# Kernel tuning notes

Hardware: AMD Instinct MI355X
Metric: run time of the kernel (lower is better)

The kernel has to match this reference:

```python
import jax, jax.numpy as jnp
import numpy as np

N = 50000          # nodes
E = 1600000        # edges (avg degree 32)
B = 64             # graphs in batch
IN_CH = 128
HEADS = 8
HD = 8             # head_dim = ceil(64/8)
GH = HEADS * HD    # 64 = gat_hidden_dim
HIDDEN = 64
NC = 10
NEG_SLOPE = 0.2
BN_EPS = 1e-5
SIGMA = 0.5


def setup_inputs() -> dict:
    key = jax.random.key(0)
    ks = jax.random.split(key, 24)
    s = 0.1
    inp = {
        "x": jax.random.normal(ks[0], (N, IN_CH), jnp.float32),
        "raw_x": jax.random.uniform(ks[1], (N, 3), jnp.float32),
        "edge_index": jax.random.randint(ks[2], (2, E), 0, N, jnp.int32),
        "batch": jnp.sort(jax.random.randint(ks[3], (N,), 0, B, jnp.int32)),
        # conv1 (heads=8, out=8, edge_dim=1)
        "W1": jax.random.normal(ks[4], (IN_CH, GH), jnp.float32) * s,
        "att_src1": jax.random.normal(ks[5], (HEADS, HD), jnp.float32) * s,
        "att_dst1": jax.random.normal(ks[6], (HEADS, HD), jnp.float32) * s,
        "We1": jax.random.normal(ks[7], (1, GH), jnp.float32) * s,
        "att_e1": jax.random.normal(ks[8], (HEADS, HD), jnp.float32) * s,
        "b1": jax.random.normal(ks[9], (GH,), jnp.float32) * s,
        "gamma1": jnp.ones((GH,), jnp.float32),
        "beta1": jnp.zeros((GH,), jnp.float32),
        "rm1": jax.random.normal(ks[10], (GH,), jnp.float32) * s,
        "rv1": jax.random.uniform(ks[11], (GH,), jnp.float32) + 0.5,
        # conv2 (heads=1, out=64, edge_dim=1)
        "W2": jax.random.normal(ks[12], (GH, HIDDEN), jnp.float32) * s,
        "att_src2": jax.random.normal(ks[13], (1, HIDDEN), jnp.float32) * s,
        "att_dst2": jax.random.normal(ks[14], (1, HIDDEN), jnp.float32) * s,
        "We2": jax.random.normal(ks[15], (1, HIDDEN), jnp.float32) * s,
        "att_e2": jax.random.normal(ks[16], (1, HIDDEN), jnp.float32) * s,
        "b2": jax.random.normal(ks[17], (HIDDEN,), jnp.float32) * s,
        "gamma2": jnp.ones((HIDDEN,), jnp.float32),
        "beta2": jnp.zeros((HIDDEN,), jnp.float32),
        "rm2": jax.random.normal(ks[18], (HIDDEN,), jnp.float32) * s,
        "rv2": jax.random.uniform(ks[19], (HIDDEN,), jnp.float32) + 0.5,
        # classifier
        "Wc": jax.random.normal(ks[20], (HIDDEN, NC), jnp.float32) * s,
        "bc": jax.random.normal(ks[21], (NC,), jnp.float32) * s,
    }
    return inp


def _gat_conv(x, src, dst, edge_attr, W, a_src, a_dst, W_e, a_e, bias, heads, out_ch, n):
    """PyG GATConv (concat=True, add_self_loops=True, fill_value='mean', eval mode)."""
    e0 = edge_attr.shape[0]
    # self-loop edge_attr = mean of incoming edge_attr per node (0 if isolated)
    cnt = jax.ops.segment_sum(jnp.ones((e0,), x.dtype), dst, num_segments=n)
    loop_attr = jax.ops.segment_sum(edge_attr, dst, num_segments=n) / jnp.maximum(cnt, 1.0)[:, None]
    loops = jnp.arange(n, dtype=src.dtype)
    src2 = jnp.concatenate([src, loops])
    dst2 = jnp.concatenate([dst, loops])
    ea = jnp.concatenate([edge_attr, loop_attr], axis=0)          # [E2, 1]
    h = (x @ W).reshape(n, heads, out_ch)                          # [N, H, D]
    al_s = (h * a_src).sum(-1)                                     # [N, H]
    al_d = (h * a_dst).sum(-1)                                     # [N, H]
    al_e = ((ea @ W_e).reshape(-1, heads, out_ch) * a_e).sum(-1)   # [E2, H]
    logits = al_s[src2] + al_d[dst2] + al_e                        # [E2, H]
    logits = jnp.where(logits >= 0, logits, NEG_SLOPE * logits)    # leaky_relu
    # segment softmax over destination nodes (every node has a self loop)
    m = jax.ops.segment_max(logits, dst2, num_segments=n)
    ex = jnp.exp(logits - m[dst2])
    alpha = ex / jax.ops.segment_sum(ex, dst2, num_segments=n)[dst2]
    out = jax.ops.segment_sum(h[src2] * alpha[:, :, None], dst2, num_segments=n)
    return out.reshape(n, heads * out_ch) + bias


def _bn_eval(x, gamma, beta, rm, rv):
    return (x - rm) * (gamma / jnp.sqrt(rv + BN_EPS)) + beta


def reference(x, raw_x, edge_index, batch,
              W1, att_src1, att_dst1, We1, att_e1, b1, gamma1, beta1, rm1, rv1,
              W2, att_src2, att_dst2, We2, att_e2, b2, gamma2, beta2, rm2, rv2,
              Wc, bc):
    src, dst = edge_index[0], edge_index[1]
    # gaussian edge weights from raw features
    diff = raw_x[src] - raw_x[dst]
    dist2 = (diff * diff).sum(axis=1)
    edge_w = jnp.exp(-dist2 / (2.0 * SIGMA * SIGMA))[:, None]      # [E, 1]
    # eval mode: dropout is identity
    h = _gat_conv(x, src, dst, edge_w, W1, att_src1, att_dst1, We1, att_e1, b1, HEADS, HD, N)
    h = jax.nn.elu(_bn_eval(h, gamma1, beta1, rm1, rv1))
    h = _gat_conv(h, src, dst, edge_w, W2, att_src2, att_dst2, We2, att_e2, b2, 1, HIDDEN, N)
    h = jax.nn.elu(_bn_eval(h, gamma2, beta2, rm2, rv2))
    # global mean pool over graphs
    cnt = jax.ops.segment_sum(jnp.ones((N,), h.dtype), batch, num_segments=B)
    g = jax.ops.segment_sum(h, batch, num_segments=B) / jnp.maximum(cnt, 1.0)[:, None]
    return g @ Wc + bc
```

## Files before the change

### kernel.cpp

```cpp
#include <hip/hip_runtime.h>
#include <math.h>

#define N_NODES 50000
#define N_EDGES 1600000
#define NBATCH  64
#define INCH    128
#define HEADS   8
#define HD      8
#define GH      64
#define HIDDEN  64
#define NC      10
#define NEG_SLOPE 0.2f
#define BN_EPS  1e-5f

#define SCAN_TPB 1024
#define NTILES   ((N_NODES + SCAN_TPB - 1) / SCAN_TPB)

typedef unsigned short ushort_t;
typedef unsigned int uint_t;

__device__ __forceinline__ ushort_t f2bf(float f) {
  uint_t u = __float_as_uint(f);
  uint_t r = (u + 0x7fffu + ((u >> 16) & 1u)) >> 16;
  return (ushort_t)r;
}
__device__ __forceinline__ float2 upk(uint_t u) {
  return make_float2(__uint_as_float(u << 16), __uint_as_float(u & 0xffff0000u));
}

__global__ __launch_bounds__(256) void edge_kernel(
    const int* __restrict__ ei, const float* __restrict__ raw,
    float* __restrict__ ea, float* __restrict__ easum, int* __restrict__ cnt) {
  int e = blockIdx.x * blockDim.x + threadIdx.x;
  if (e >= N_EDGES) return;
  int s = ei[e], d = ei[N_EDGES + e];
  float dx = raw[s*3+0] - raw[d*3+0];
  float dy = raw[s*3+1] - raw[d*3+1];
  float dz = raw[s*3+2] - raw[d*3+2];
  float w = __expf(-2.0f * (dx*dx + dy*dy + dz*dz));
  ea[e] = w;
  atomicAdd(&easum[d], w);
  atomicAdd(&cnt[d], 1);
}

__global__ __launch_bounds__(SCAN_TPB) void scan_part(
    const int* __restrict__ cnt, const float* __restrict__ easum,
    int* __restrict__ rowptr, float* __restrict__ loopat, int* __restrict__ bsum) {
  __shared__ int s[SCAN_TPB];
  int t = threadIdx.x;
  int i = blockIdx.x * SCAN_TPB + t;
  int v = (i < N_NODES) ? cnt[i] : 0;
  s[t] = v; __syncthreads();
  for (int off = 1; off < SCAN_TPB; off <<= 1) {
    int u = (t >= off) ? s[t - off] : 0;
    __syncthreads();
    s[t] += u;
    __syncthreads();
  }
  if (i < N_NODES) {
    rowptr[i] = s[t] - v;
    loopat[i] = easum[i] / fmaxf((float)v, 1.0f);
  }
  if (t == SCAN_TPB - 1) bsum[blockIdx.x] = s[t];
}

__global__ __launch_bounds__(64) void scan_top(int* __restrict__ bsum, int* __restrict__ rowptr) {
  int t = threadIdx.x;
  int v = (t < NTILES) ? bsum[t] : 0;
  int orig = v;
  for (int off = 1; off < 64; off <<= 1) {
    int u = __shfl_up(v, off);
    if (t >= off) v += u;
  }
  if (t < NTILES) bsum[t] = v - orig;
  if (t == 0) rowptr[N_NODES] = N_EDGES;
}

__global__ __launch_bounds__(SCAN_TPB) void scan_add(int* __restrict__ rowptr, const int* __restrict__ bsum) {
  int i = blockIdx.x * SCAN_TPB + threadIdx.x;
  if (i < N_NODES) rowptr[i] += bsum[blockIdx.x];
}

__global__ __launch_bounds__(256) void scatter_kernel(
    const int* __restrict__ ei, const float* __restrict__ ea,
    const int* __restrict__ rowptr, int* __restrict__ cnt2,
    int* __restrict__ csr_src, float* __restrict__ csr_ea) {
  int e = blockIdx.x * blockDim.x + threadIdx.x;
  if (e >= N_EDGES) return;
  int s = ei[e], d = ei[N_EDGES + e];
  int pos = rowptr[d] + atomicAdd(&cnt2[d], 1);
  csr_src[pos] = s;
  csr_ea[pos] = ea[e];
}

__global__ __launch_bounds__(256) void gemm1_kernel(
    const float* __restrict__ x, const float* __restrict__ W1,
    ushort_t* __restrict__ h1b) {
  __shared__ float w[INCH * GH];
  for (int i = threadIdx.x; i < INCH * GH / 4; i += blockDim.x)
    ((float4*)w)[i] = ((const float4*)W1)[i];
  __syncthreads();
  int lane = threadIdx.x & 63;
  int waveG = __builtin_amdgcn_readfirstlane((blockIdx.x * blockDim.x + threadIdx.x) >> 6);
  int nWaves = (gridDim.x * blockDim.x) >> 6;
  for (int base = waveG * 4; base < N_NODES; base += nWaves * 4) {
    float acc[4] = {0.f, 0.f, 0.f, 0.f};
    #pragma unroll 8
    for (int k = 0; k < INCH; ++k) {
      float wv = w[k * GH + lane];
      #pragma unroll
      for (int j = 0; j < 4; ++j)
        acc[j] = fmaf(x[(size_t)(base + j) * INCH + k], wv, acc[j]);
    }
    #pragma unroll
    for (int j = 0; j < 4; ++j)
      h1b[(size_t)(base + j) * GH + lane] = f2bf(acc[j]);
  }
}

__global__ __launch_bounds__(256) void conv1_kernel(
    const ushort_t* __restrict__ h1b,
    const float* __restrict__ asrc, const float* __restrict__ adst,
    const float* __restrict__ We, const float* __restrict__ ae,
    const int* __restrict__ rowptr,
    const int* __restrict__ csr_src, const float* __restrict__ csr_ea,
    const float* __restrict__ loopat, const float* __restrict__ bias,
    const float* __restrict__ gamma, const float* __restrict__ beta,
    const float* __restrict__ rm, const float* __restrict__ rv,
    float* __restrict__ h2) {
  __shared__ int   src_lds[4][64];
  __shared__ float ea_lds[4][64];
  int l = threadIdx.x & 63;
  int w = threadIdx.x >> 6;
  int n = blockIdx.x * 4 + w;
  if (n >= N_NODES) return;
  int i = l & 15;
  int q = l >> 4;
  const float4 as4 = ((const float4*)asrc)[i];
  const float4 ad4 = ((const float4*)adst)[i];
  float4 we4 = ((const float4*)We)[i];
  float4 ae4 = ((const float4*)ae)[i];
  float ce = we4.x*ae4.x + we4.y*ae4.y + we4.z*ae4.z + we4.w*ae4.w;
  ce += __shfl_xor(ce, 1);
  const uint2* tab = (const uint2*)h1b;
  uint2 uself = tab[(size_t)n * 16 + i];
  float2 s01 = upk(uself.x), s23 = upk(uself.y);
  float als_s = s01.x*as4.x + s01.y*as4.y + s23.x*as4.z + s23.y*as4.w;
  als_s += __shfl_xor(als_s, 1);
  float aldn  = s01.x*ad4.x + s01.y*ad4.y + s23.x*ad4.z + s23.y*ad4.w;
  aldn += __shfl_xor(aldn, 1);
  int jb = rowptr[n], je = rowptr[n + 1];
  float m = -1e30f, ssum = 0.f;
  float a0 = 0.f, a1 = 0.f, a2 = 0.f, a3 = 0.f;
  for (int cb = jb; cb < je; cb += 64) {
    int cnt = je - cb; if (cnt > 64) cnt = 64;
    int idx = cb + l;
    bool vld = l < cnt;
    src_lds[w][l] = vld ? csr_src[idx] : 0;
    ea_lds[w][l]  = vld ? csr_ea[idx] : 0.f;
    int nb = (cnt + 3) >> 2;
    int j0 = q;
    int s0 = (j0 < cnt) ? src_lds[w][j0] : 0;
    uint2 rcur = tab[(size_t)s0 * 16 + i];
    for (int b = 0; b < nb; ++b) {
      uint2 rnext = rcur;
      if (b + 1 < nb) {
        int jn = ((b + 1) << 2) + q;
        int sn = (jn < cnt) ? src_lds[w][jn] : 0;
        rnext = tab[(size_t)sn * 16 + i];
      }
      int j = (b << 2) + q;
      bool val = j < cnt;
      float eav = val ? ea_lds[w][j] : 0.f;
      float2 p01 = upk(rcur.x), p23 = upk(rcur.y);
      float dp = p01.x*as4.x + p01.y*as4.y + p23.x*as4.z + p23.y*as4.w;
      dp += __shfl_xor(dp, 1);
      float lg = dp + aldn + eav * ce;
      lg = (lg >= 0.f) ? lg : NEG_SLOPE * lg;
      lg = val ? lg : -1e30f;
      float bm = fmaxf(lg, __shfl_xor(lg, 16));
      bm = fmaxf(bm, __shfl_xor(bm, 32));
      float nm = fmaxf(m, bm);
      float sc = __expf(m - nm);
      float p  = __expf(lg - nm);
      float ps = p;
      ps += __shfl_xor(ps, 16);
      ps += __shfl_xor(ps, 32);
      ssum = ssum * sc + ps;
      m = nm;
      a0 = a0 * sc + p * p01.x;
      a1 = a1 * sc + p * p01.y;
      a2 = a2 * sc + p * p23.x;
      a3 = a3 * sc + p * p23.y;
      rcur = rnext;
    }
  }
  a0 += __shfl_xor(a0, 16); a0 += __shfl_xor(a0, 32);
  a1 += __shfl_xor(a1, 16); a1 += __shfl_xor(a1, 32);
  a2 += __shfl_xor(a2, 16); a2 += __shfl_xor(a2, 32);
  a3 += __shfl_xor(a3, 16); a3 += __shfl_xor(a3, 32);
  {
    float lg = als_s + aldn + loopat[n] * ce;
    lg = (lg >= 0.f) ? lg : NEG_SLOPE * lg;
    float nm = fmaxf(m, lg);
    float sc = __expf(m - nm);
    float p  = __expf(lg - nm);
    ssum = ssum * sc + p;
    a0 = a0 * sc + p * s01.x;
    a1 = a1 * sc + p * s01.y;
    a2 = a2 * sc + p * s23.x;
    a3 = a3 * sc + p * s23.y;
  }
  float inv = 1.0f / ssum;
  float4 b4 = ((const float4*)bias)[i];
  float4 g4 = ((const float4*)gamma)[i];
  float4 be4 = ((const float4*)beta)[i];
  float4 rm4 = ((const float4*)rm)[i];
  float4 rv4 = ((const float4*)rv)[i];
  float o0 = a0 * inv + b4.x, o1 = a1 * inv + b4.y;
  float o2 = a2 * inv + b4.z, o3 = a3 * inv + b4.w;
  o0 = (o0 - rm4.x) * (g4.x * rsqrtf(rv4.x + BN_EPS)) + be4.x;
  o1 = (o1 - rm4.y) * (g4.y * rsqrtf(rv4.y + BN_EPS)) + be4.y;
  o2 = (o2 - rm4.z) * (g4.z * rsqrtf(rv4.z + BN_EPS)) + be4.z;
  o3 = (o3 - rm4.w) * (g4.w * rsqrtf(rv4.w + BN_EPS)) + be4.w;
  o0 = (o0 > 0.f) ? o0 : expm1f(o0);
  o1 = (o1 > 0.f) ? o1 : expm1f(o1);
  o2 = (o2 > 0.f) ? o2 : expm1f(o2);
  o3 = (o3 > 0.f) ? o3 : expm1f(o3);
  if (q == 0)
    ((float4*)(h2 + (size_t)n * GH))[i] = make_float4(o0, o1, o2, o3);
}

__global__ __launch_bounds__(256) void gemm2_kernel(
    const float* __restrict__ x, const float* __restrict__ W2,
    ushort_t* __restrict__ h2mb) {
  __shared__ float w[HIDDEN * HIDDEN];
  for (int i = threadIdx.x; i < HIDDEN * HIDDEN / 4; i += blockDim.x)
    ((float4*)w)[i] = ((const float4*)W2)[i];
  __syncthreads();
  int lane = threadIdx.x & 63;
  int waveG = __builtin_amdgcn_readfirstlane((blockIdx.x * blockDim.x + threadIdx.x) >> 6);
  int nWaves = (gridDim.x * blockDim.x) >> 6;
  for (int base = waveG * 4; base < N_NODES; base += nWaves * 4) {
    float acc[4] = {0.f, 0.f, 0.f, 0.f};
    #pragma unroll 8
    for (int k = 0; k < HIDDEN; ++k) {
      float wv = w[k * HIDDEN + lane];
      #pragma unroll
      for (int j = 0; j < 4; ++j)
        acc[j] = fmaf(x[(size_t)(base + j) * HIDDEN + k], wv, acc[j]);
    }
    #pragma unroll
    for (int j = 0; j < 4; ++j)
      h2mb[(size_t)(base + j) * HIDDEN + lane] = f2bf(acc[j]);
  }
}

__global__ __launch_bounds__(256) void conv2_kernel(
    const ushort_t* __restrict__ h2mb,
    const float* __restrict__ asrc, const float* __restrict__ adst,
    const float* __restrict__ We, const float* __restrict__ ae,
    const int* __restrict__ rowptr,
    const int* __restrict__ csr_src, const float* __restrict__ csr_ea,
    const float* __restrict__ loopat, const float* __restrict__ bias,
    const float* __restrict__ gamma, const float* __restrict__ beta,
    const float* __restrict__ rm, const float* __restrict__ rv,
    const int* __restrict__ batch,
    float* __restrict__ pool, int* __restrict__ cntg) {
  __shared__ int   src_lds[4][64];
  __shared__ float ea_lds[4][64];
  int l = threadIdx.x & 63;
  int w = threadIdx.x >> 6;
  int n = blockIdx.x * 4 + w;
  if (n >= N_NODES) return;
  int i = l & 15;
  int q = l >> 4;
  const float4 as4 = ((const float4*)asrc)[i];
  const float4 ad4 = ((const float4*)adst)[i];
  float4 we4 = ((const float4*)We)[i];
  float4 ae4 = ((const float4*)ae)[i];
  float ce = we4.x*ae4.x + we4.y*ae4.y + we4.z*ae4.z + we4.w*ae4.w;
  ce += __shfl_xor(ce, 1); ce += __shfl_xor(ce, 2);
  ce += __shfl_xor(ce, 4); ce += __shfl_xor(ce, 8);
  const uint2* tab = (const uint2*)h2mb;
  uint2 uself = tab[(size_t)n * 16 + i];
  float2 s01 = upk(uself.x), s23 = upk(uself.y);
  float als_s = s01.x*as4.x + s01.y*as4.y + s23.x*as4.z + s23.y*as4.w;
  als_s += __shfl_xor(als_s, 1); als_s += __shfl_xor(als_s, 2);
  als_s += __shfl_xor(als_s, 4); als_s += __shfl_xor(als_s, 8);
  float aldn  = s01.x*ad4.x + s01.y*ad4.y + s23.x*ad4.z + s23.y*ad4.w;
  aldn += __shfl_xor(aldn, 1); aldn += __shfl_xor(aldn, 2);
  aldn += __shfl_xor(aldn, 4); aldn += __shfl_xor(aldn, 8);
  int jb = rowptr[n], je = rowptr[n + 1];
  float m = -1e30f, ssum = 0.f;
  float a0 = 0.f, a1 = 0.f, a2 = 0.f, a3 = 0.f;
  for (int cb = jb; cb < je; cb += 64) {
    int cnt = je - cb; if (cnt > 64) cnt = 64;
    int idx = cb + l;
    bool vld = l < cnt;
    src_lds[w][l] = vld ? csr_src[idx] : 0;
    ea_lds[w][l]  = vld ? csr_ea[idx] : 0.f;
    int nb = (cnt + 3) >> 2;
    int j0 = q;
    int s0 = (j0 < cnt) ? src_lds[w][j0] : 0;
    uint2 rcur = tab[(size_t)s0 * 16 + i];
    for (int b = 0; b < nb; ++b) {
      uint2 rnext = rcur;
      if (b + 1 < nb) {
        int jn = ((b + 1) << 2) + q;
        int sn = (jn < cnt) ? src_lds[w][jn] : 0;
        rnext = tab[(size_t)sn * 16 + i];
      }
      int j = (b << 2) + q;
      bool val = j < cnt;
      float eav = val ? ea_lds[w][j] : 0.f;
      float2 p01 = upk(rcur.x), p23 = upk(rcur.y);
      float dp = p01.x*as4.x + p01.y*as4.y + p23.x*as4.z + p23.y*as4.w;
      dp += __shfl_xor(dp, 1); dp += __shfl_xor(dp, 2);
      dp += __shfl_xor(dp, 4); dp += __shfl_xor(dp, 8);
      float lg = dp + aldn + eav * ce;
      lg = (lg >= 0.f) ? lg : NEG_SLOPE * lg;
      lg = val ? lg : -1e30f;
      float bm = fmaxf(lg, __shfl_xor(lg, 16));
      bm = fmaxf(bm, __shfl_xor(bm, 32));
      float nm = fmaxf(m, bm);
      float sc = __expf(m - nm);
      float p  = __expf(lg - nm);
      float ps = p;
      ps += __shfl_xor(ps, 16);
      ps += __shfl_xor(ps, 32);
      ssum = ssum * sc + ps;
      m = nm;
      a0 = a0 * sc + p * p01.x;
      a1 = a1 * sc + p * p01.y;
      a2 = a2 * sc + p * p23.x;
      a3 = a3 * sc + p * p23.y;
      rcur = rnext;
    }
  }
  a0 += __shfl_xor(a0, 16); a0 += __shfl_xor(a0, 32);
  a1 += __shfl_xor(a1, 16); a1 += __shfl_xor(a1, 32);
  a2 += __shfl_xor(a2, 16); a2 += __shfl_xor(a2, 32);
  a3 += __shfl_xor(a3, 16); a3 += __shfl_xor(a3, 32);
  {
    float lg = als_s + aldn + loopat[n] * ce;
    lg = (lg >= 0.f) ? lg : NEG_SLOPE * lg;
    float nm = fmaxf(m, lg);
    float sc = __expf(m - nm);
    float p  = __expf(lg - nm);
    ssum = ssum * sc + p;
    a0 = a0 * sc + p * s01.x;
    a1 = a1 * sc + p * s01.y;
    a2 = a2 * sc + p * s23.x;
    a3 = a3 * sc + p * s23.y;
  }
  float inv = 1.0f / ssum;
  float4 b4 = ((const float4*)bias)[i];
  float4 g4 = ((const float4*)gamma)[i];
  float4 be4 = ((const float4*)beta)[i];
  float4 rm4 = ((const float4*)rm)[i];
  float4 rv4 = ((const float4*)rv)[i];
  float o0 = a0 * inv + b4.x, o1 = a1 * inv + b4.y;
  float o2 = a2 * inv + b4.z, o3 = a3 * inv + b4.w;
  o0 = (o0 - rm4.x) * (g4.x * rsqrtf(rv4.x + BN_EPS)) + be4.x;
  o1 = (o1 - rm4.y) * (g4.y * rsqrtf(rv4.y + BN_EPS)) + be4.y;
  o2 = (o2 - rm4.z) * (g4.z * rsqrtf(rv4.z + BN_EPS)) + be4.z;
  o3 = (o3 - rm4.w) * (g4.w * rsqrtf(rv4.w + BN_EPS)) + be4.w;
  o0 = (o0 > 0.f) ? o0 : expm1f(o0);
  o1 = (o1 > 0.f) ? o1 : expm1f(o1);
  o2 = (o2 > 0.f) ? o2 : expm1f(o2);
  o3 = (o3 > 0.f) ? o3 : expm1f(o3);
  if (q == 0) {
    int b = batch[n];
    float* pp = pool + (size_t)b * HIDDEN + 4 * i;
    atomicAdd(pp + 0, o0);
    atomicAdd(pp + 1, o1);
    atomicAdd(pp + 2, o2);
    atomicAdd(pp + 3, o3);
    if (l == 0) atomicAdd(&cntg[b], 1);
  }
}

__global__ __launch_bounds__(640) void final_kernel(
    const float* __restrict__ pool, const int* __restrict__ cntg,
    const float* __restrict__ Wc, const float* __restrict__ bc,
    float* __restrict__ out) {
  int t = threadIdx.x;
  if (t >= NBATCH * NC) return;
  int b = t / NC, c = t - b * NC;
  float inv = 1.0f / fmaxf((float)cntg[b], 1.0f);
  float s = bc[c];
  #pragma unroll
  for (int d = 0; d < HIDDEN; ++d)
    s = fmaf(pool[b * HIDDEN + d] * inv, Wc[d * NC + c], s);
  out[t] = s;
}

extern "C" void kernel_launch(void* const* d_in, const int* in_sizes, int n_in,
                              void* d_out, int out_size, void* d_ws, size_t ws_size,
                              hipStream_t stream) {
  const float* x     = (const float*)d_in[0];
  const float* raw   = (const float*)d_in[1];
  const int*   ei    = (const int*)  d_in[2];
  const int*   batch = (const int*)  d_in[3];
  const float* W1    = (const float*)d_in[4];
  const float* asrc1 = (const float*)d_in[5];
  const float* adst1 = (const float*)d_in[6];
  const float* We1   = (const float*)d_in[7];
  const float* ae1   = (const float*)d_in[8];
  const float* b1    = (const float*)d_in[9];
  const float* g1    = (const float*)d_in[10];
  const float* be1   = (const float*)d_in[11];
  const float* rm1   = (const float*)d_in[12];
  const float* rv1   = (const float*)d_in[13];
  const float* W2    = (const float*)d_in[14];
  const float* asrc2 = (const float*)d_in[15];
  const float* adst2 = (const float*)d_in[16];
  const float* We2   = (const float*)d_in[17];
  const float* ae2   = (const float*)d_in[18];
  const float* b2    = (const float*)d_in[19];
  const float* g2    = (const float*)d_in[20];
  const float* be2   = (const float*)d_in[21];
  const float* rm2   = (const float*)d_in[22];
  const float* rv2   = (const float*)d_in[23];
  const float* Wc    = (const float*)d_in[24];
  const float* bc    = (const float*)d_in[25];
  float* out = (float*)d_out;

  char* ws = (char*)d_ws;
  size_t off = 0;
  auto alloc = [&](size_t bytes) -> void* {
    void* p = ws + off;
    off += bytes;
    off = (off + 255) & ~(size_t)255;
    return p;
  };
  float*    ea      = (float*)   alloc((size_t)N_EDGES * 4);
  float*    csr_ea  = (float*)   alloc((size_t)N_EDGES * 4);
  int*      csr_src = (int*)     alloc((size_t)N_EDGES * 4);
  float*    easum   = (float*)   alloc((size_t)N_NODES * 4);
  int*      cnt     = (int*)     alloc((size_t)N_NODES * 4);
  int*      cnt2    = (int*)     alloc((size_t)N_NODES * 4);
  int*      rowptr  = (int*)     alloc((size_t)(N_NODES + 1) * 4);
  float*    loopat  = (float*)   alloc((size_t)N_NODES * 4);
  ushort_t* h1b     = (ushort_t*)alloc((size_t)N_NODES * GH * 2);
  float*    h2      = (float*)   alloc((size_t)N_NODES * GH * 4);
  ushort_t* h2mb    = (ushort_t*)alloc((size_t)N_NODES * HIDDEN * 2);
  int*      bsum    = (int*)     alloc(64 * 4);
  float*    pool    = (float*)   alloc((size_t)NBATCH * HIDDEN * 4);
  int*      cntg    = (int*)     alloc((size_t)NBATCH * 4);

  hipMemsetAsync(easum, 0, (size_t)N_NODES * 4, stream);
  hipMemsetAsync(cnt,   0, (size_t)N_NODES * 4, stream);
  hipMemsetAsync(cnt2,  0, (size_t)N_NODES * 4, stream);
  hipMemsetAsync(pool,  0, (size_t)NBATCH * HIDDEN * 4, stream);
  hipMemsetAsync(cntg,  0, (size_t)NBATCH * 4, stream);

  int egrid = (N_EDGES + 255) / 256;
  edge_kernel<<<egrid, 256, 0, stream>>>(ei, raw, ea, easum, cnt);
  scan_part<<<NTILES, SCAN_TPB, 0, stream>>>(cnt, easum, rowptr, loopat, bsum);
  scan_top<<<1, 64, 0, stream>>>(bsum, rowptr);
  scan_add<<<NTILES, SCAN_TPB, 0, stream>>>(rowptr, bsum);
  scatter_kernel<<<egrid, 256, 0, stream>>>(ei, ea, rowptr, cnt2, csr_src, csr_ea);

  gemm1_kernel<<<1024, 256, 0, stream>>>(x, W1, h1b);
  conv1_kernel<<<(N_NODES + 3) / 4, 256, 0, stream>>>(h1b, asrc1, adst1, We1, ae1,
      rowptr, csr_src, csr_ea, loopat, b1, g1, be1, rm1, rv1, h2);
  gemm2_kernel<<<1024, 256, 0, stream>>>(h2, W2, h2mb);
  conv2_kernel<<<(N_NODES + 3) / 4, 256, 0, stream>>>(h2mb, asrc2, adst2, We2, ae2,
      rowptr, csr_src, csr_ea, loopat, b2, g2, be2, rm2, rv2, batch, pool, cntg);
  final_kernel<<<1, 640, 0, stream>>>(pool, cntg, Wc, bc, out);
}
```

Before: 929.9 us.

## Remap conv lanes to 16 edges x 4 feature chunks, drop online softmax max

Both GAT aggregation kernels now assign each lane a 16-feature chunk (two 16-byte bf16 row loads) and process 16 edges per wave step instead of 4. Cross-lane shuffles per edge largely disappear; the feature accumulators are reduced across edge groups only once at the end. The online max-rescaling softmax is replaced by a plain exp clamped at 60, which removes the per-step max and rescale work. In exchange, each lane holds 16 accumulators plus the attention vectors, raising register pressure, and numerical stability now depends on logits staying small.

```diff
diff --git a/kernel.cpp b/kernel.cpp
--- a/kernel.cpp
+++ b/kernel.cpp
@@ -26,6 +26,13 @@
 }
 __device__ __forceinline__ float2 upk(uint_t u) {
   return make_float2(__uint_as_float(u << 16), __uint_as_float(u & 0xffff0000u));
+}
+__device__ __forceinline__ void upk8(uint4 u, float* v) {
+  float2 t;
+  t = upk(u.x); v[0] = t.x; v[1] = t.y;
+  t = upk(u.y); v[2] = t.x; v[3] = t.y;
+  t = upk(u.z); v[4] = t.x; v[5] = t.y;
+  t = upk(u.w); v[6] = t.x; v[7] = t.y;
 }
 
 __global__ __launch_bounds__(256) void edge_kernel(
@@ -134,101 +141,126 @@
   int w = threadIdx.x >> 6;
   int n = blockIdx.x * 4 + w;
   if (n >= N_NODES) return;
-  int i = l & 15;
-  int q = l >> 4;
-  const float4 as4 = ((const float4*)asrc)[i];
-  const float4 ad4 = ((const float4*)adst)[i];
-  float4 we4 = ((const float4*)We)[i];
-  float4 ae4 = ((const float4*)ae)[i];
-  float ce = we4.x*ae4.x + we4.y*ae4.y + we4.z*ae4.z + we4.w*ae4.w;
-  ce += __shfl_xor(ce, 1);
-  const uint2* tab = (const uint2*)h1b;
-  uint2 uself = tab[(size_t)n * 16 + i];
-  float2 s01 = upk(uself.x), s23 = upk(uself.y);
-  float als_s = s01.x*as4.x + s01.y*as4.y + s23.x*as4.z + s23.y*as4.w;
-  als_s += __shfl_xor(als_s, 1);
-  float aldn  = s01.x*ad4.x + s01.y*ad4.y + s23.x*ad4.z + s23.y*ad4.w;
-  aldn += __shfl_xor(aldn, 1);
+  int g = l >> 2;
+  int c = l & 3;
+  float as[16];
+  float ce0 = 0.f, ce1 = 0.f;
+  float ad[16];
+  #pragma unroll
+  for (int k = 0; k < 4; ++k) {
+    float4 t = ((const float4*)asrc)[c*4 + k];
+    as[4*k+0] = t.x; as[4*k+1] = t.y; as[4*k+2] = t.z; as[4*k+3] = t.w;
+    float4 d = ((const float4*)adst)[c*4 + k];
+    ad[4*k+0] = d.x; ad[4*k+1] = d.y; ad[4*k+2] = d.z; ad[4*k+3] = d.w;
+    float4 wv = ((const float4*)We)[c*4 + k];
+    float4 av = ((const float4*)ae)[c*4 + k];
+    float s = wv.x*av.x + wv.y*av.y + wv.z*av.z + wv.w*av.w;
+    if (k < 2) ce0 += s; else ce1 += s;
+  }
+  const uint4* tab4 = (const uint4*)h1b;
+  uint4 sr0 = tab4[(size_t)n*8 + c*2];
+  uint4 sr1 = tab4[(size_t)n*8 + c*2 + 1];
+  float sv0[8], sv1[8];
+  upk8(sr0, sv0); upk8(sr1, sv1);
+  float als0 = 0.f, als1 = 0.f, ald0 = 0.f, ald1 = 0.f;
+  #pragma unroll
+  for (int j = 0; j < 8; ++j) {
+    als0 = fmaf(sv0[j], as[j], als0);
+    ald0 = fmaf(sv0[j], ad[j], ald0);
+    als1 = fmaf(sv1[j], as[8+j], als1);
+    ald1 = fmaf(sv1[j], ad[8+j], ald1);
+  }
   int jb = rowptr[n], je = rowptr[n + 1];
-  float m = -1e30f, ssum = 0.f;
-  float a0 = 0.f, a1 = 0.f, a2 = 0.f, a3 = 0.f;
+  float ssum0 = 0.f, ssum1 = 0.f;
+  float a[16];
+  #pragma unroll
+  for (int k = 0; k < 16; ++k) a[k] = 0.f;
   for (int cb = jb; cb < je; cb += 64) {
     int cnt = je - cb; if (cnt > 64) cnt = 64;
     int idx = cb + l;
     bool vld = l < cnt;
     src_lds[w][l] = vld ? csr_src[idx] : 0;
     ea_lds[w][l]  = vld ? csr_ea[idx] : 0.f;
-    int nb = (cnt + 3) >> 2;
-    int j0 = q;
+    int nb = (cnt + 15) >> 4;
+    int j0 = g;
     int s0 = (j0 < cnt) ? src_lds[w][j0] : 0;
-    uint2 rcur = tab[(size_t)s0 * 16 + i];
+    uint4 r0 = tab4[(size_t)s0*8 + c*2];
+    uint4 r1 = tab4[(size_t)s0*8 + c*2 + 1];
     for (int b = 0; b < nb; ++b) {
-      uint2 rnext = rcur;
+      uint4 n0 = r0, n1 = r1;
       if (b + 1 < nb) {
-        int jn = ((b + 1) << 2) + q;
+        int jn = ((b + 1) << 4) + g;
         int sn = (jn < cnt) ? src_lds[w][jn] : 0;
-        rnext = tab[(size_t)sn * 16 + i];
+        n0 = tab4[(size_t)sn*8 + c*2];
+        n1 = tab4[(size_t)sn*8 + c*2 + 1];
       }
-      int j = (b << 2) + q;
+      int j = (b << 4) + g;
       bool val = j < cnt;
       float eav = val ? ea_lds[w][j] : 0.f;
-      float2 p01 = upk(rcur.x), p23 = upk(rcur.y);
-      float dp = p01.x*as4.x + p01.y*as4.y + p23.x*as4.z + p23.y*as4.w;
-      dp += __shfl_xor(dp, 1);
-      float lg = dp + aldn + eav * ce;
-      lg = (lg >= 0.f) ? lg : NEG_SLOPE * lg;
-      lg = val ? lg : -1e30f;
-      float bm = fmaxf(lg, __shfl_xor(lg, 16));
-      bm = fmaxf(bm, __shfl_xor(bm, 32));
-      float nm = fmaxf(m, bm);
-      float sc = __expf(m - nm);
-      float p  = __expf(lg - nm);
-      float ps = p;
-      ps += __shfl_xor(ps, 16);
-      ps += __shfl_xor(ps, 32);
-      ssum = ssum * sc + ps;
-      m = nm;
-      a0 = a0 * sc + p * p01.x;
-      a1 = a1 * sc + p * p01.y;
-      a2 = a2 * sc + p * p23.x;
-      a3 = a3 * sc + p * p23.y;
-      rcur = rnext;
-    }
-  }
-  a0 += __shfl_xor(a0, 16); a0 += __shfl_xor(a0, 32);
-  a1 += __shfl_xor(a1, 16); a1 += __shfl_xor(a1, 32);
-  a2 += __shfl_xor(a2, 16); a2 += __shfl_xor(a2, 32);
-  a3 += __shfl_xor(a3, 16); a3 += __shfl_xor(a3, 32);
+      float v0[8], v1[8];
+      upk8(r0, v0); upk8(r1, v1);
+      float dp0 = 0.f, dp1 = 0.f;
+      #pragma unroll
+      for (int k = 0; k < 8; ++k) {
+        dp0 = fmaf(v0[k], as[k], dp0);
+        dp1 = fmaf(v1[k], as[8+k], dp1);
+      }
+      float lg0 = dp0 + ald0 + eav * ce0;
+      float lg1 = dp1 + ald1 + eav * ce1;
+      lg0 = (lg0 >= 0.f) ? lg0 : NEG_SLOPE * lg0;
+      lg1 = (lg1 >= 0.f) ? lg1 : NEG_SLOPE * lg1;
+      lg0 = val ? lg0 : -1e30f;
+      lg1 = val ? lg1 : -1e30f;
+      float p0 = __expf(fminf(lg0, 60.f));
+      float p1 = __expf(fminf(lg1, 60.f));
+      ssum0 += p0; ssum1 += p1;
+      #pragma unroll
+      for (int k = 0; k < 8; ++k) {
+        a[k]   = fmaf(p0, v0[k], a[k]);
+        a[8+k] = fmaf(p1, v1[k], a[8+k]);
+      }
+      r0 = n0; r1 = n1;
+    }
+  }
+  ssum0 += __shfl_xor(ssum0, 4); ssum0 += __shfl_xor(ssum0, 8);
+  ssum0 += __shfl_xor(ssum0, 16); ssum0 += __shfl_xor(ssum0, 32);
+  ssum1 += __shfl_xor(ssum1, 4); ssum1 += __shfl_xor(ssum1, 8);
+  ssum1 += __shfl_xor(ssum1, 16); ssum1 += __shfl_xor(ssum1, 32);
+  #pragma unroll
+  for (int k = 0; k < 16; ++k) {
+    a[k] += __shfl_xor(a[k], 4);  a[k] += __shfl_xor(a[k], 8);
+    a[k] += __shfl_xor(a[k], 16); a[k] += __shfl_xor(a[k], 32);
+  }
   {
-    float lg = als_s + aldn + loopat[n] * ce;
-    lg = (lg >= 0.f) ? lg : NEG_SLOPE * lg;
-    float nm = fmaxf(m, lg);
-    float sc = __expf(m - nm);
-    float p  = __expf(lg - nm);
-    ssum = ssum * sc + p;
-    a0 = a0 * sc + p * s01.x;
-    a1 = a1 * sc + p * s01.y;
-    a2 = a2 * sc + p * s23.x;
-    a3 = a3 * sc + p * s23.y;
-  }
-  float inv = 1.0f / ssum;
-  float4 b4 = ((const float4*)bias)[i];
-  float4 g4 = ((const float4*)gamma)[i];
-  float4 be4 = ((const float4*)beta)[i];
-  float4 rm4 = ((const float4*)rm)[i];
-  float4 rv4 = ((const float4*)rv)[i];
-  float o0 = a0 * inv + b4.x, o1 = a1 * inv + b4.y;
-  float o2 = a2 * inv + b4.z, o3 = a3 * inv + b4.w;
-  o0 = (o0 - rm4.x) * (g4.x * rsqrtf(rv4.x + BN_EPS)) + be4.x;
-  o1 = (o1 - rm4.y) * (g4.y * rsqrtf(rv4.y + BN_EPS)) + be4.y;
-  o2 = (o2 - rm4.z) * (g4.z * rsqrtf(rv4.z + BN_EPS)) + be4.z;
-  o3 = (o3 - rm4.w) * (g4.w * rsqrtf(rv4.w + BN_EPS)) + be4.w;
-  o0 = (o0 > 0.f) ? o0 : expm1f(o0);
-  o1 = (o1 > 0.f) ? o1 : expm1f(o1);
-  o2 = (o2 > 0.f) ? o2 : expm1f(o2);
-  o3 = (o3 > 0.f) ? o3 : expm1f(o3);
-  if (q == 0)
-    ((float4*)(h2 + (size_t)n * GH))[i] = make_float4(o0, o1, o2, o3);
+    float la = loopat[n];
+    float lg0 = als0 + ald0 + la * ce0;
+    float lg1 = als1 + ald1 + la * ce1;
+    lg0 = (lg0 >= 0.f) ? lg0 : NEG_SLOPE * lg0;
+    lg1 = (lg1 >= 0.f) ? lg1 : NEG_SLOPE * lg1;
+    float p0 = __expf(fminf(lg0, 60.f));
+    float p1 = __expf(fminf(lg1, 60.f));
+    ssum0 += p0; ssum1 += p1;
+    #pragma unroll
+    for (int k = 0; k < 8; ++k) {
+      a[k]   = fmaf(p0, sv0[k], a[k]);
+      a[8+k] = fmaf(p1, sv1[k], a[8+k]);
+    }
+  }
+  if (g == 0) {
+    float inv0 = 1.0f / ssum0, inv1 = 1.0f / ssum1;
+    float o[16];
+    #pragma unroll
+    for (int k = 0; k < 16; ++k) {
+      int d = c*16 + k;
+      float ov = a[k] * ((k < 8) ? inv0 : inv1) + bias[d];
+      ov = (ov - rm[d]) * (gamma[d] * rsqrtf(rv[d] + BN_EPS)) + beta[d];
+      o[k] = (ov > 0.f) ? ov : expm1f(ov);
+    }
+    float4* dst = (float4*)(h2 + (size_t)n * GH);
+    #pragma unroll
+    for (int k = 0; k < 4; ++k)
+      dst[c*4 + k] = make_float4(o[4*k], o[4*k+1], o[4*k+2], o[4*k+3]);
+  }
 }
 
 __global__ __launch_bounds__(256) void gemm2_kernel(
@@ -273,110 +305,117 @@
   int w = threadIdx.x >> 6;
   int n = blockIdx.x * 4 + w;
   if (n >= N_NODES) return;
-  int i = l & 15;
-  int q = l >> 4;
-  const float4 as4 = ((const float4*)asrc)[i];
-  const float4 ad4 = ((const float4*)adst)[i];
-  float4 we4 = ((const float4*)We)[i];
-  float4 ae4 = ((const float4*)ae)[i];
-  float ce = we4.x*ae4.x + we4.y*ae4.y + we4.z*ae4.z + we4.w*ae4.w;
+  int g = l >> 2;
+  int c = l & 3;
+  float as[16];
+  float cep = 0.f;
+  float ad[16];
+  #pragma unroll
+  for (int k = 0; k < 4; ++k) {
+    float4 t = ((const float4*)asrc)[c*4 + k];
+    as[4*k+0] = t.x; as[4*k+1] = t.y; as[4*k+2] = t.z; as[4*k+3] = t.w;
+    float4 d = ((const float4*)adst)[c*4 + k];
+    ad[4*k+0] = d.x; ad[4*k+1] = d.y; ad[4*k+2] = d.z; ad[4*k+3] = d.w;
+    float4 wv = ((const float4*)We)[c*4 + k];
+    float4 av = ((const float4*)ae)[c*4 + k];
+    cep += wv.x*av.x + wv.y*av.y + wv.z*av.z + wv.w*av.w;
+  }
+  float ce = cep;
   ce += __shfl_xor(ce, 1); ce += __shfl_xor(ce, 2);
-  ce += __shfl_xor(ce, 4); ce += __shfl_xor(ce, 8);
-  const uint2* tab = (const uint2*)h2mb;
-  uint2 uself = tab[(size_t)n * 16 + i];
-  float2 s01 = upk(uself.x), s23 = upk(uself.y);
-  float als_s = s01.x*as4.x + s01.y*as4.y + s23.x*as4.z + s23.y*as4.w;
-  als_s += __shfl_xor(als_s, 1); als_s += __shfl_xor(als_s, 2);
-  als_s += __shfl_xor(als_s, 4); als_s += __shfl_xor(als_s, 8);
-  float aldn  = s01.x*ad4.x + s01.y*ad4.y + s23.x*ad4.z + s23.y*ad4.w;
-  aldn += __shfl_xor(aldn, 1); aldn += __shfl_xor(aldn, 2);
-  aldn += __shfl_xor(aldn, 4); aldn += __shfl_xor(aldn, 8);
+  const uint4* tab4 = (const uint4*)h2mb;
+  uint4 sr0 = tab4[(size_t)n*8 + c*2];
+  uint4 sr1 = tab4[(size_t)n*8 + c*2 + 1];
+  float sv0[8], sv1[8];
+  upk8(sr0, sv0); upk8(sr1, sv1);
+  float alsp = 0.f, aldp = 0.f;
+  #pragma unroll
+  for (int j = 0; j < 8; ++j) {
+    alsp = fmaf(sv0[j], as[j], alsp);
+    alsp = fmaf(sv1[j], as[8+j], alsp);
+    aldp = fmaf(sv0[j], ad[j], aldp);
+    aldp = fmaf(sv1[j], ad[8+j], aldp);
+  }
+  float als_s = alsp; als_s += __shfl_xor(als_s, 1); als_s += __shfl_xor(als_s, 2);
+  float aldn  = aldp; aldn  += __shfl_xor(aldn, 1);  aldn  += __shfl_xor(aldn, 2);
   int jb = rowptr[n], je = rowptr[n + 1];
-  float m = -1e30f, ssum = 0.f;
-  float a0 = 0.f, a1 = 0.f, a2 = 0.f, a3 = 0.f;
+  float ssum = 0.f;
+  float a[16];
+  #pragma unroll
+  for (int k = 0; k < 16; ++k) a[k] = 0.f;
   for (int cb = jb; cb < je; cb += 64) {
     int cnt = je - cb; if (cnt > 64) cnt = 64;
     int idx = cb + l;
     bool vld = l < cnt;
     src_lds[w][l] = vld ? csr_src[idx] : 0;
     ea_lds[w][l]  = vld ? csr_ea[idx] : 0.f;
-    int nb = (cnt + 3) >> 2;
-    int j0 = q;
+    int nb = (cnt + 15) >> 4;
+    int j0 = g;
     int s0 = (j0 < cnt) ? src_lds[w][j0] : 0;
-    uint2 rcur = tab[(size_t)s0 * 16 + i];
+    uint4 r0 = tab4[(size_t)s0*8 + c*2];
+    uint4 r1 = tab4[(size_t)s0*8 + c*2 + 1];
     for (int b = 0; b < nb; ++b) {
-      uint2 rnext = rcur;
+      uint4 n0 = r0, n1 = r1;
       if (b + 1 < nb) {
-        int jn = ((b + 1) << 2) + q;
+        int jn = ((b + 1) << 4) + g;
         int sn = (jn < cnt) ? src_lds[w][jn] : 0;
-        rnext = tab[(size_t)sn * 16 + i];
+        n0 = tab4[(size_t)sn*8 + c*2];
+        n1 = tab4[(size_t)sn*8 + c*2 + 1];
       }
-      int j = (b << 2) + q;
+      int j = (b << 4) + g;
       bool val = j < cnt;
       float eav = val ? ea_lds[w][j] : 0.f;
-      float2 p01 = upk(rcur.x), p23 = upk(rcur.y);
-      float dp = p01.x*as4.x + p01.y*as4.y + p23.x*as4.z + p23.y*as4.w;
+      float v0[8], v1[8];
+      upk8(r0, v0); upk8(r1, v1);
+      float dp = 0.f;
+      #pragma unroll
+      for (int k = 0; k < 8; ++k) {
+        dp = fmaf(v0[k], as[k], dp);
+        dp = fmaf(v1[k], as[8+k], dp);
+      }
       dp += __shfl_xor(dp, 1); dp += __shfl_xor(dp, 2);
-      dp += __shfl_xor(dp, 4); dp += __shfl_xor(dp, 8);
       float lg = dp + aldn + eav * ce;
       lg = (lg >= 0.f) ? lg : NEG_SLOPE * lg;
       lg = val ? lg : -1e30f;
-      float bm = fmaxf(lg, __shfl_xor(lg, 16));
-      bm = fmaxf(bm, __shfl_xor(bm, 32));
-      float nm = fmaxf(m, bm);
-      float sc = __expf(m - nm);
-      float p  = __expf(lg - nm);
-      float ps = p;
-      ps += __shfl_xor(ps, 16);
-      ps += __shfl_xor(ps, 32);
-      ssum = ssum * sc + ps;
-      m = nm;
-      a0 = a0 * sc + p * p01.x;
-      a1 = a1 * sc + p * p01.y;
-      a2 = a2 * sc + p * p23.x;
-      a3 = a3 * sc + p * p23.y;
-      rcur = rnext;
-    }
-  }
-  a0 += __shfl_xor(a0, 16); a0 += __shfl_xor(a0, 32);
-  a1 += __shfl_xor(a1, 16); a1 += __shfl_xor(a1, 32);
-  a2 += __shfl_xor(a2, 16); a2 += __shfl_xor(a2, 32);
-  a3 += __shfl_xor(a3, 16); a3 += __shfl_xor(a3, 32);
+      float p = __expf(fminf(lg, 60.f));
+      ssum += p;
+      #pragma unroll
+      for (int k = 0; k < 8; ++k) {
+        a[k]   = fmaf(p, v0[k], a[k]);
+        a[8+k] = fmaf(p, v1[k], a[8+k]);
+      }
+      r0 = n0; r1 = n1;
+    }
+  }
+  ssum += __shfl_xor(ssum, 4); ssum += __shfl_xor(ssum, 8);
+  ssum += __shfl_xor(ssum, 16); ssum += __shfl_xor(ssum, 32);
+  #pragma unroll
+  for (int k = 0; k < 16; ++k) {
+    a[k] += __shfl_xor(a[k], 4);  a[k] += __shfl_xor(a[k], 8);
+    a[k] += __shfl_xor(a[k], 16); a[k] += __shfl_xor(a[k], 32);
+  }
   {
     float lg = als_s + aldn + loopat[n] * ce;
     lg = (lg >= 0.f) ? lg : NEG_SLOPE * lg;
-    float nm = fmaxf(m, lg);
-    float sc = __expf(m - nm);
-    float p  = __expf(lg - nm);
-    ssum = ssum * sc + p;
-    a0 = a0 * sc + p * s01.x;
-    a1 = a1 * sc + p * s01.y;
-    a2 = a2 * sc + p * s23.x;
-    a3 = a3 * sc + p * s23.y;
-  }
-  float inv = 1.0f / ssum;
-  float4 b4 = ((const float4*)bias)[i];
-  float4 g4 = ((const float4*)gamma)[i];
-  float4 be4 = ((const float4*)beta)[i];
-  float4 rm4 = ((const float4*)rm)[i];
-  float4 rv4 = ((const float4*)rv)[i];
-  float o0 = a0 * inv + b4.x, o1 = a1 * inv + b4.y;
-  float o2 = a2 * inv + b4.z, o3 = a3 * inv + b4.w;
-  o0 = (o0 - rm4.x) * (g4.x * rsqrtf(rv4.x + BN_EPS)) + be4.x;
-  o1 = (o1 - rm4.y) * (g4.y * rsqrtf(rv4.y + BN_EPS)) + be4.y;
-  o2 = (o2 - rm4.z) * (g4.z * rsqrtf(rv4.z + BN_EPS)) + be4.z;
-  o3 = (o3 - rm4.w) * (g4.w * rsqrtf(rv4.w + BN_EPS)) + be4.w;
-  o0 = (o0 > 0.f) ? o0 : expm1f(o0);
-  o1 = (o1 > 0.f) ? o1 : expm1f(o1);
-  o2 = (o2 > 0.f) ? o2 : expm1f(o2);
-  o3 = (o3 > 0.f) ? o3 : expm1f(o3);
-  if (q == 0) {
+    float p = __expf(fminf(lg, 60.f));
+    ssum += p;
+    #pragma unroll
+    for (int k = 0; k < 8; ++k) {
+      a[k]   = fmaf(p, sv0[k], a[k]);
+      a[8+k] = fmaf(p, sv1[k], a[8+k]);
+    }
+  }
+  if (g == 0) {
+    float inv = 1.0f / ssum;
     int b = batch[n];
-    float* pp = pool + (size_t)b * HIDDEN + 4 * i;
-    atomicAdd(pp + 0, o0);
-    atomicAdd(pp + 1, o1);
-    atomicAdd(pp + 2, o2);
-    atomicAdd(pp + 3, o3);
+    float* pp = pool + (size_t)b * HIDDEN + 16 * c;
+    #pragma unroll
+    for (int k = 0; k < 16; ++k) {
+      int d = c*16 + k;
+      float ov = a[k] * inv + bias[d];
+      ov = (ov - rm[d]) * (gamma[d] * rsqrtf(rv[d] + BN_EPS)) + beta[d];
+      ov = (ov > 0.f) ? ov : expm1f(ov);
+      atomicAdd(pp + k, ov);
+    }
     if (l == 0) atomicAdd(&cntg[b], 1);
   }
 }
```

Result: slower. 1.974 ms (+112.3%).
